# Kernel optimization log

Measured on AMD Instinct MI355X. Metric: run time of the kernel, lower is better.

The kernel has to match this reference:

```python
import jax, jax.numpy as jnp
import numpy as np

N_NODES = 64
KS = (52, 42, 34)  # ceil(0.8*64), ceil(0.8*52), ceil(0.8*42)


def _gcn(x, A, W, b):
    # GCNConv(improved=True): self-loop fill 2.0, symmetric normalization. A[tgt, src], weighted.
    n = A.shape[0]
    Ah = A + 2.0 * jnp.eye(n, dtype=A.dtype)
    d = Ah.sum(-1)
    dis = jnp.where(d > 0, jax.lax.rsqrt(d), 0.0)
    An = dis[:, None] * Ah * dis[None, :]
    return An @ (x @ W) + b


def _augment(A):
    # GraphUNet.augment_adj: add self loops (weight 1), A2 = A1 @ A1, remove self loops
    n = A.shape[0]
    eye = jnp.eye(n, dtype=A.dtype)
    A1 = A + eye
    return (A1 @ A1) * (1.0 - eye)


def _pool(x, A, w, k):
    # TopKPooling: score = tanh(x.w/||w||), keep top-k, scale kept features by score
    s = jnp.tanh((x @ w) / jnp.linalg.norm(w))
    sv, perm = jax.lax.top_k(s, k)
    return x[perm] * sv[:, None], A[perm][:, perm], perm


def _unet(x, A, dw0, db0, dws, dbs, pws, uws, ubs, uwl, ubl):
    # GraphUNet(depth=3, sum_res=True), single graph: x [n, F2], A [n, n]
    x = jax.nn.relu(_gcn(x, A, dw0, db0))
    xs, As, perms = [x], [A], []
    for i in range(3):
        A = _augment(A)
        x, A, perm = _pool(x, A, pws[i], KS[i])
        x = jax.nn.relu(_gcn(x, A, dws[i], dbs[i]))
        if i < 2:
            xs.append(x)
            As.append(A)
        perms.append(perm)
    for i in range(3):
        j = 2 - i
        res, Aj, perm = xs[j], As[j], perms[j]
        x = res + jnp.zeros_like(res).at[perm].set(x)
        if i < 2:
            x = jax.nn.relu(_gcn(x, Aj, uws[i], ubs[i]))
        else:
            x = _gcn(x, Aj, uwl, ubl)
    return x


def _nnconv(x, src, dst, ea, mw, mb, rw, bias):
    # NNConv(aggr='mean'): per-edge MLP weight, gather-matmul-scatter-mean + root + bias
    B, E = src.shape
    fin, fout = rw.shape
    We = jax.nn.relu(ea @ mw + mb).reshape(B, E, fin, fout)  # [B,E,fin,fout]
    xs = jnp.take_along_axis(x, src[..., None], axis=1)      # [B,E,fin]
    msg = jnp.einsum('bei,beio->beo', xs, We)                # [B,E,fout]
    seg = jax.vmap(lambda m, d: jax.ops.segment_sum(m, d, num_segments=N_NODES))
    sums = seg(msg, dst)
    cnt = seg(jnp.ones(msg.shape[:2] + (1,), msg.dtype), dst)
    agg = sums / jnp.maximum(cnt, 1.0)
    return agg + x @ rw + bias


def _adj(src, dst):
    A = jnp.zeros((N_NODES, N_NODES), jnp.float32).at[dst, src].set(1.0)
    return A * (1.0 - jnp.eye(N_NODES, dtype=jnp.float32))


def _branch(x, ei, ea, mlp1, mlp2, u1, u2):
    src, dst = ei[:, 0], ei[:, 1]
    A = jax.vmap(_adj)(src, dst)
    x = jax.nn.relu(_nnconv(x, src, dst, ea, *mlp1))
    x = jax.nn.relu(jax.vmap(lambda h, a: _unet(h, a, *u1))(x, A))
    x = jax.nn.relu(_nnconv(x, src, dst, ea, *mlp2))
    x = jax.nn.relu(jax.vmap(lambda h, a: _unet(h, a, *u2))(x, A))
    return x.mean(axis=1)  # global_mean_pool (equal-sized graphs)


def setup_inputs() -> dict:
    key = jax.random.key(0)
    keys = iter(jax.random.split(key, 64))
    def nrm(shape, s=1.0):
        return jax.random.normal(next(keys), shape, jnp.float32) * s
    B, n, E, F, F2, Q, H, C = 128, 64, 512, 64, 32, 16, 256, 50
    inp = {}
    inp['x1'] = nrm((B, n, F))
    inp['ei1'] = jax.random.randint(next(keys), (B, 2, E), 0, n, jnp.int32)
    inp['ea1'] = jax.random.uniform(next(keys), (B, E, 1), jnp.float32)
    inp['jw1'] = nrm((B, Q))
    inp['x2'] = nrm((B, n, F))
    inp['ei2'] = jax.random.randint(next(keys), (B, 2, E), 0, n, jnp.int32)
    inp['ea2'] = jax.random.uniform(next(keys), (B, E, 1), jnp.float32)
    inp['jw2'] = nrm((B, Q))
    inp['m1w'] = nrm((1, F * F2), 0.1)
    inp['m1b'] = nrm((F * F2,), 0.1)
    inp['r1w'] = nrm((F, F2), 0.1)
    inp['c1b'] = nrm((F2,), 0.1)
    inp['m2w'] = nrm((1, F2 * F2), 0.1)
    inp['m2b'] = nrm((F2 * F2,), 0.1)
    inp['r2w'] = nrm((F2, F2), 0.1)
    inp['c2b'] = nrm((F2,), 0.1)
    for p in ('u1', 'u2'):
        inp[p + '_dw0'] = nrm((F2, C), 0.1)
        inp[p + '_db0'] = nrm((C,), 0.1)
        inp[p + '_dws'] = nrm((3, C, C), 0.1)
        inp[p + '_dbs'] = nrm((3, C), 0.1)
        inp[p + '_pws'] = nrm((3, C), 0.1)
        inp[p + '_uws'] = nrm((2, C, C), 0.1)
        inp[p + '_ubs'] = nrm((2, C), 0.1)
        inp[p + '_uwl'] = nrm((C, F2), 0.1)
        inp[p + '_ubl'] = nrm((F2,), 0.1)
    inp['bb_w'] = nrm(((F2 + Q) * 2, H), 0.1)
    inp['bb_b'] = nrm((H,), 0.1)
    return inp


def reference(x1, ei1, ea1, jw1, x2, ei2, ea2, jw2,
              m1w, m1b, r1w, c1b, m2w, m2b, r2w, c2b,
              u1_dw0, u1_db0, u1_dws, u1_dbs, u1_pws, u1_uws, u1_ubs, u1_uwl, u1_ubl,
              u2_dw0, u2_db0, u2_dws, u2_dbs, u2_pws, u2_uws, u2_ubs, u2_uwl, u2_ubl,
              bb_w, bb_b):
    mlp1 = (m1w, m1b, r1w, c1b)
    mlp2 = (m2w, m2b, r2w, c2b)
    u1 = (u1_dw0, u1_db0, u1_dws, u1_dbs, u1_pws, u1_uws, u1_ubs, u1_uwl, u1_ubl)
    u2 = (u2_dw0, u2_db0, u2_dws, u2_dbs, u2_pws, u2_uws, u2_ubs, u2_uwl, u2_ubl)
    r1 = _branch(x1, ei1, ea1, mlp1, mlp2, u1, u2)
    r2 = _branch(x2, ei2, ea2, mlp1, mlp2, u1, u2)
    c = jnp.concatenate([r1, jw1, r2, jw2], axis=1)  # [(F2+Q)*2]
    return jax.nn.relu(c @ bb_w + bb_b)
```

## Files before the change

kernel.cpp:

```cpp
#include <hip/hip_runtime.h>
#include <math.h>

#define UT 1024
#define XS 52
#define ASTR 65

__device__ __forceinline__ float wred16(float v) {
    v += __shfl_xor(v, 8); v += __shfl_xor(v, 4);
    v += __shfl_xor(v, 2); v += __shfl_xor(v, 1);
    return v;
}

__global__ __launch_bounds__(256)
void adj_kernel(const int* __restrict__ eiA, const int* __restrict__ eiB,
                float* __restrict__ Aout)
{
    const int g = blockIdx.x, tid = threadIdx.x;
    const int* eig = (g < 128) ? (eiA + (size_t)g * 1024)
                               : (eiB + (size_t)(g - 128) * 1024);
    __shared__ float Al[4096];
    for (int i = tid; i < 4096; i += 256) Al[i] = 0.f;
    __syncthreads();
    for (int e = tid; e < 512; e += 256) {
        int s = eig[e], d = eig[512 + e];
        Al[d * 64 + s] = 1.f;
    }
    __syncthreads();
    if (tid < 64) Al[tid * 64 + tid] = 0.f;
    __syncthreads();
    for (int i = tid; i < 4096; i += 256) Aout[(size_t)g * 4096 + i] = Al[i];
}

template<int FIN>
__global__ __launch_bounds__(UT)
void nnconv_kernel(const float* __restrict__ xA, const float* __restrict__ xB,
                   const int* __restrict__ eiA, const int* __restrict__ eiB,
                   const float* __restrict__ eaA, const float* __restrict__ eaB,
                   const float* __restrict__ mw, const float* __restrict__ mb,
                   const float* __restrict__ rw, const float* __restrict__ bias,
                   float* __restrict__ out)
{
    constexpr int ICN = FIN / 16;
    constexpr int ERN = UT / (32 * ICN);
    constexpr int EPT = 512 / ERN;
    const int g = blockIdx.x, tid = threadIdx.x;
    const float* xg; const int* eig; const float* eag;
    if (g < 128) {
        xg = xA + (size_t)g * 64 * FIN; eig = eiA + (size_t)g * 1024; eag = eaA + (size_t)g * 512;
    } else {
        int h = g - 128;
        xg = xB + (size_t)h * 64 * FIN; eig = eiB + (size_t)h * 1024; eag = eaB + (size_t)h * 512;
    }

    __shared__ __align__(16) float xl[64 * FIN];
    __shared__ __align__(16) float mwl[FIN * 32];
    __shared__ __align__(16) float mbl[FIN * 32];
    __shared__ __align__(16) float rwl[FIN * 32];
    __shared__ __align__(16) float sums[64 * 32];
    __shared__ int   srcl[512];
    __shared__ int   dstl[512];
    __shared__ float eal[512];
    __shared__ float cntl[64];

    for (int i = tid; i < 64 * FIN; i += UT) xl[i] = xg[i];
    for (int i = tid; i < FIN * 32; i += UT) { mwl[i] = mw[i]; mbl[i] = mb[i]; rwl[i] = rw[i]; }
    for (int e = tid; e < 512; e += UT) {
        srcl[e] = eig[e]; dstl[e] = eig[512 + e]; eal[e] = eag[e];
    }
    for (int i = tid; i < 2048; i += UT) sums[i] = 0.f;
    if (tid < 64) cntl[tid] = 0.f;
    __syncthreads();

    const int o = tid & 31, ic = (tid >> 5) & (ICN - 1), er = tid / (32 * ICN);
    float mwr[16], mbr[16];
    #pragma unroll
    for (int z = 0; z < 16; z++) {
        mwr[z] = mwl[(ic * 16 + z) * 32 + o];
        mbr[z] = mbl[(ic * 16 + z) * 32 + o];
    }
    for (int e = tid; e < 512; e += UT) atomicAdd(&cntl[dstl[e]], 1.f);

    for (int e = er * EPT; e < er * EPT + EPT; e++) {
        int s = srcl[e]; int d = dstl[e]; float av = eal[e];
        float acc = 0.f;
        #pragma unroll
        for (int z = 0; z < 16; z += 4) {
            float4 xv = *(const float4*)&xl[s * FIN + ic * 16 + z];
            acc += xv.x * fmaxf(fmaf(av, mwr[z + 0], mbr[z + 0]), 0.f);
            acc += xv.y * fmaxf(fmaf(av, mwr[z + 1], mbr[z + 1]), 0.f);
            acc += xv.z * fmaxf(fmaf(av, mwr[z + 2], mbr[z + 2]), 0.f);
            acc += xv.w * fmaxf(fmaf(av, mwr[z + 3], mbr[z + 3]), 0.f);
        }
        acc += __shfl_down(acc, 32);
        if ((tid & 32) == 0) atomicAdd(&sums[d * 32 + o], acc);
    }
    __syncthreads();

    for (int it = tid; it < 512; it += UT) {
        int nn = it >> 3, o0 = (it & 7) * 4;
        float a0 = 0.f, a1 = 0.f, a2 = 0.f, a3 = 0.f;
        for (int i = 0; i < FIN; i++) {
            float xv = xl[nn * FIN + i];
            float4 w = *(const float4*)&rwl[i * 32 + o0];
            a0 = fmaf(xv, w.x, a0); a1 = fmaf(xv, w.y, a1);
            a2 = fmaf(xv, w.z, a2); a3 = fmaf(xv, w.w, a3);
        }
        float inv = 1.0f / fmaxf(cntl[nn], 1.f);
        float4 sv = *(const float4*)&sums[nn * 32 + o0];
        float4 bv = *(const float4*)&bias[o0];
        float4 r;
        r.x = fmaxf(sv.x * inv + a0 + bv.x, 0.f);
        r.y = fmaxf(sv.y * inv + a1 + bv.y, 0.f);
        r.z = fmaxf(sv.z * inv + a2 + bv.z, 0.f);
        r.w = fmaxf(sv.w * inv + a3 + bv.w, 0.f);
        *(float4*)&out[(size_t)g * 2048 + nn * 32 + o0] = r;
    }
}

__device__ __forceinline__ void gcn_u(int n, int cin, int cout,
    float* __restrict__ x, float* __restrict__ tmp,
    const float* __restrict__ A, float* __restrict__ Wl,
    float* __restrict__ dis,
    const float* __restrict__ Wg, const float* __restrict__ bg, bool relu)
{
    const int tid = threadIdx.x;
    const int nso = (cout + 3) >> 2;
    for (int idx = tid; idx < 51 * 52; idx += UT) {
        int r = idx / 52, c = idx - r * 52;
        float v = 0.f;
        if (r < cin && c < cout) v = Wg[r * cout + c];
        else if (r == 50 && c < cout) v = bg[c];
        Wl[idx] = v;
    }
    {
        int r = tid >> 4, l = tid & 15;
        float s = 0.f;
        if (r < n) for (int j = l; j < n; j += 16) s += A[r * ASTR + j];
        s = wred16(s);
        if (l == 0 && r < n) dis[r] = 1.0f / sqrtf(2.0f + s);
    }
    __syncthreads();
    int nr2 = n >> 1;
    for (int it = tid; it < nr2 * nso; it += UT) {
        int i0 = (it / nso) * 2, o0 = (it - (it / nso) * nso) * 4;
        float a0=0,a1=0,a2=0,a3=0, b0=0,b1=0,b2=0,b3=0;
        for (int k = 0; k < cin; k++) {
            float4 w = *(const float4*)&Wl[k * 52 + o0];
            float x0 = x[i0 * XS + k], x1 = x[(i0 + 1) * XS + k];
            a0 = fmaf(x0, w.x, a0); a1 = fmaf(x0, w.y, a1);
            a2 = fmaf(x0, w.z, a2); a3 = fmaf(x0, w.w, a3);
            b0 = fmaf(x1, w.x, b0); b1 = fmaf(x1, w.y, b1);
            b2 = fmaf(x1, w.z, b2); b3 = fmaf(x1, w.w, b3);
        }
        float d0 = dis[i0], d1 = dis[i0 + 1];
        float4 t0; t0.x = a0*d0; t0.y = a1*d0; t0.z = a2*d0; t0.w = a3*d0;
        float4 t1; t1.x = b0*d1; t1.y = b1*d1; t1.z = b2*d1; t1.w = b3*d1;
        *(float4*)&tmp[i0 * XS + o0] = t0;
        *(float4*)&tmp[(i0 + 1) * XS + o0] = t1;
    }
    __syncthreads();
    for (int it = tid; it < nr2 * nso; it += UT) {
        int i0 = (it / nso) * 2, o0 = (it - (it / nso) * nso) * 4;
        float a0=0,a1=0,a2=0,a3=0, b0=0,b1=0,b2=0,b3=0;
        for (int j = 0; j < n; j++) {
            float4 t = *(const float4*)&tmp[j * XS + o0];
            float av0 = A[i0 * ASTR + j], av1 = A[(i0 + 1) * ASTR + j];
            a0 = fmaf(av0, t.x, a0); a1 = fmaf(av0, t.y, a1);
            a2 = fmaf(av0, t.z, a2); a3 = fmaf(av0, t.w, a3);
            b0 = fmaf(av1, t.x, b0); b1 = fmaf(av1, t.y, b1);
            b2 = fmaf(av1, t.z, b2); b3 = fmaf(av1, t.w, b3);
        }
        float4 bias = *(const float4*)&Wl[50 * 52 + o0];
        float4 s0 = *(const float4*)&tmp[i0 * XS + o0];
        float4 s1 = *(const float4*)&tmp[(i0 + 1) * XS + o0];
        float d0 = dis[i0], d1 = dis[i0 + 1];
        float4 r0, r1;
        r0.x = fmaf(d0, a0 + 2.f*s0.x, bias.x); r0.y = fmaf(d0, a1 + 2.f*s0.y, bias.y);
        r0.z = fmaf(d0, a2 + 2.f*s0.z, bias.z); r0.w = fmaf(d0, a3 + 2.f*s0.w, bias.w);
        r1.x = fmaf(d1, b0 + 2.f*s1.x, bias.x); r1.y = fmaf(d1, b1 + 2.f*s1.y, bias.y);
        r1.z = fmaf(d1, b2 + 2.f*s1.z, bias.z); r1.w = fmaf(d1, b3 + 2.f*s1.w, bias.w);
        if (relu) {
            r0.x = fmaxf(r0.x, 0.f); r0.y = fmaxf(r0.y, 0.f);
            r0.z = fmaxf(r0.z, 0.f); r0.w = fmaxf(r0.w, 0.f);
            r1.x = fmaxf(r1.x, 0.f); r1.y = fmaxf(r1.y, 0.f);
            r1.z = fmaxf(r1.z, 0.f); r1.w = fmaxf(r1.w, 0.f);
        }
        *(float4*)&x[i0 * XS + o0] = r0;
        *(float4*)&x[(i0 + 1) * XS + o0] = r1;
    }
    __syncthreads();
}

__global__ __launch_bounds__(UT)
void unet_kernel(const float* __restrict__ xin, const float* __restrict__ Aglob,
                 const float* __restrict__ dw0, const float* __restrict__ db0,
                 const float* __restrict__ dws, const float* __restrict__ dbs,
                 const float* __restrict__ pws,
                 const float* __restrict__ uws, const float* __restrict__ ubs,
                 const float* __restrict__ uwl, const float* __restrict__ ubl,
                 float* __restrict__ ws_xs, float* __restrict__ ws_As,
                 float* __restrict__ outp, int mean_mode)
{
    const int g = blockIdx.x, tid = threadIdx.x;
    __shared__ __align__(16) float Aa[64 * ASTR];
    __shared__ __align__(16) float Ab[64 * ASTR];
    __shared__ __align__(16) float x0c[64 * XS];
    __shared__ __align__(16) float x1c[64 * XS];
    __shared__ float scr[64];
    __shared__ float dis[64];
    __shared__ float svals[64];
    __shared__ int   permL[192];

    float *pA = Aa, *pF = Ab, *px = x0c, *pt_ = x1c;
    float* xs_g = ws_xs + (size_t)g * 9984;
    float* as_g = ws_As + (size_t)g * 6144;
    const float* Ag_g = Aglob + (size_t)g * 4096;
    const int nsz[4] = {64, 52, 42, 34};

    {
        const float* xg = xin + (size_t)g * 2048;
        for (int idx = tid; idx < 512; idx += UT) {
            int i = idx >> 3, o0 = (idx & 7) * 4;
            *(float4*)&px[i * XS + o0] = *(const float4*)&xg[i * 32 + o0];
        }
        for (int idx = tid; idx < 4096; idx += UT)
            pA[(idx >> 6) * ASTR + (idx & 63)] = Ag_g[idx];
    }
    __syncthreads();

    gcn_u(64, 32, 50, px, pt_, pA, pF, dis, dw0, db0, true);

    for (int lvl = 0; lvl < 3; lvl++) {
        int n = nsz[lvl], kk = nsz[lvl + 1];
        const float* wg = pws + lvl * 50;
        int* perm = permL + lvl * 64;
        {
            int r = tid >> 4, l = tid & 15;
            float s = 0.f, wn = 0.f;
            for (int q = l; q < 50; q += 16) {
                float wv = wg[q];
                wn = fmaf(wv, wv, wn);
                s = fmaf(px[r * XS + q], wv, s);
            }
            s = wred16(s); wn = wred16(wn);
            if (l == 0 && r < n) scr[r] = tanhf(s / sqrtf(wn));
        }
        {
            float* xd = xs_g + lvl * 3328;
            for (int idx = tid; idx < 3328; idx += UT) xd[idx] = px[idx];
            if (lvl == 1) for (int idx = tid; idx < 52 * ASTR; idx += UT) as_g[idx] = pA[idx];
            if (lvl == 2) for (int idx = tid; idx < 42 * ASTR; idx += UT) as_g[3380 + idx] = pA[idx];
        }
        __syncthreads();
        if (tid < 64) {
            float v = (tid < n) ? scr[tid] : -2.0f;
            int id = tid;
            for (int sz = 2; sz <= 64; sz <<= 1)
                for (int st = sz >> 1; st > 0; st >>= 1) {
                    float ov = __shfl_xor(v, st);
                    int oi = __shfl_xor(id, st);
                    bool up = ((tid & sz) == 0);
                    bool lower = ((tid & st) == 0);
                    bool less = (v > ov) || (v == ov && id < oi);
                    bool keep = (up == lower) ? less : !less;
                    if (!keep) { v = ov; id = oi; }
                }
            if (tid < kk) { perm[tid] = id; svals[tid] = v; }
        }
        __syncthreads();
        for (int idx = tid; idx < n * 13; idx += UT) {
            int m = idx / 13, u0 = (idx - (idx / 13) * 13) * 4;
            float4 gv;
            gv.x = (u0 + 0 < kk) ? pA[m * ASTR + perm[u0 + 0]] : 0.f;
            gv.y = (u0 + 1 < kk) ? pA[m * ASTR + perm[u0 + 1]] : 0.f;
            gv.z = (u0 + 2 < kk) ? pA[m * ASTR + perm[u0 + 2]] : 0.f;
            gv.w = (u0 + 3 < kk) ? pA[m * ASTR + perm[u0 + 3]] : 0.f;
            *(float4*)&pt_[m * XS + u0] = gv;
        }
        float gx0=0, gx1=0, gx2=0, gx3=0; int gdst = -1;
        if (tid < kk * 13) {
            int t = tid / 13, q0 = (tid - t * 13) * 4;
            float sv = svals[t]; int p = perm[t];
            gx0 = px[p * XS + q0 + 0] * sv; gx1 = px[p * XS + q0 + 1] * sv;
            gx2 = px[p * XS + q0 + 2] * sv; gx3 = px[p * XS + q0 + 3] * sv;
            gdst = t * XS + q0;
        }
        __syncthreads();
        if (gdst >= 0) {
            px[gdst] = gx0; px[gdst + 1] = gx1; px[gdst + 2] = gx2; px[gdst + 3] = gx3;
        }
        int nt2 = kk >> 1, nst = (kk + 3) >> 2;
        for (int it = tid; it < nt2 * nst; it += UT) {
            int t0 = (it / nst) * 2, u0 = (it - (it / nst) * nst) * 4;
            int p0 = perm[t0], p1 = perm[t0 + 1];
            float a0=0,a1=0,a2=0,a3=0, b0=0,b1=0,b2=0,b3=0;
            for (int m = 0; m < n; m++) {
                float4 gv = *(const float4*)&pt_[m * XS + u0];
                float q0v = pA[p0 * ASTR + m], q1v = pA[p1 * ASTR + m];
                a0 = fmaf(q0v, gv.x, a0); a1 = fmaf(q0v, gv.y, a1);
                a2 = fmaf(q0v, gv.z, a2); a3 = fmaf(q0v, gv.w, a3);
                b0 = fmaf(q1v, gv.x, b0); b1 = fmaf(q1v, gv.y, b1);
                b2 = fmaf(q1v, gv.z, b2); b3 = fmaf(q1v, gv.w, b3);
            }
            float4 g0 = *(const float4*)&pt_[p0 * XS + u0];
            float4 g1 = *(const float4*)&pt_[p1 * XS + u0];
            float v;
            v = a0 + 2.f*g0.x; pF[t0*ASTR + u0+0] = (u0+0 == t0) ? 0.f : v;
            v = a1 + 2.f*g0.y; pF[t0*ASTR + u0+1] = (u0+1 == t0) ? 0.f : v;
            v = a2 + 2.f*g0.z; pF[t0*ASTR + u0+2] = (u0+2 == t0) ? 0.f : v;
            v = a3 + 2.f*g0.w; pF[t0*ASTR + u0+3] = (u0+3 == t0) ? 0.f : v;
            v = b0 + 2.f*g1.x; pF[(t0+1)*ASTR + u0+0] = (u0+0 == t0+1) ? 0.f : v;
            v = b1 + 2.f*g1.y; pF[(t0+1)*ASTR + u0+1] = (u0+1 == t0+1) ? 0.f : v;
            v = b2 + 2.f*g1.z; pF[(t0+1)*ASTR + u0+2] = (u0+2 == t0+1) ? 0.f : v;
            v = b3 + 2.f*g1.w; pF[(t0+1)*ASTR + u0+3] = (u0+3 == t0+1) ? 0.f : v;
        }
        __syncthreads();
        gcn_u(kk, 50, 50, px, pt_, pF, pA, dis, dws + lvl * 2500, dbs + lvl * 50, true);
        { float* t = pA; pA = pF; pF = t; }
    }

    for (int i2 = 0; i2 < 3; i2++) {
        int j = 2 - i2;
        int nj = nsz[j], kc = nsz[j + 1];
        {
            const float* resg = xs_g + j * 3328;
            for (int idx = tid; idx < 3328; idx += UT) pt_[idx] = resg[idx];
            if (j == 0) {
                for (int idx = tid; idx < 4096; idx += UT)
                    pF[(idx >> 6) * ASTR + (idx & 63)] = Ag_g[idx];
            } else if (j == 1) {
                for (int idx = tid; idx < 52 * ASTR; idx += UT) pF[idx] = as_g[idx];
            } else {
                for (int idx = tid; idx < 42 * ASTR; idx += UT) pF[idx] = as_g[3380 + idx];
            }
        }
        __syncthreads();
        const int* perm = permL + j * 64;
        for (int it = tid; it < kc * 13; it += UT) {
            int t = it / 13, q0 = (it - (it / 13) * 13) * 4;
            int p = perm[t];
            pt_[p * XS + q0 + 0] += px[t * XS + q0 + 0];
            pt_[p * XS + q0 + 1] += px[t * XS + q0 + 1];
            pt_[p * XS + q0 + 2] += px[t * XS + q0 + 2];
            pt_[p * XS + q0 + 3] += px[t * XS + q0 + 3];
        }
        __syncthreads();
        if (i2 < 2)
            gcn_u(nj, 50, 50, pt_, px, pF, pA, dis, uws + i2 * 2500, ubs + i2 * 50, true);
        else
            gcn_u(64, 50, 32, pt_, px, pF, pA, dis, uwl, ubl, false);
        { float* t2 = px; px = pt_; pt_ = t2; }
        { float* t2 = pA; pA = pF; pF = t2; }
    }

    if (mean_mode) {
        int r = tid >> 4, l = tid & 15;
        if (r < 32) {
            float s = 0.f;
            for (int i = l; i < 64; i += 16) s += fmaxf(px[i * XS + r], 0.f);
            s = wred16(s);
            if (l == 0) outp[(size_t)g * 32 + r] = s * (1.0f / 64.0f);
        }
    } else {
        float* og = outp + (size_t)g * 2048;
        for (int idx = tid; idx < 512; idx += UT) {
            int i = idx >> 3, o0 = (idx & 7) * 4;
            float4 vv = *(const float4*)&px[i * XS + o0];
            vv.x = fmaxf(vv.x, 0.f); vv.y = fmaxf(vv.y, 0.f);
            vv.z = fmaxf(vv.z, 0.f); vv.w = fmaxf(vv.w, 0.f);
            *(float4*)&og[i * 32 + o0] = vv;
        }
    }
}

__global__ __launch_bounds__(256)
void head_kernel(const float* __restrict__ r,
                 const float* __restrict__ jw1, const float* __restrict__ jw2,
                 const float* __restrict__ bw, const float* __restrict__ bb,
                 float* __restrict__ out)
{
    const int b = blockIdx.x, h = threadIdx.x;
    float acc = bb[h];
    const float* r1 = r + (size_t)b * 32;
    const float* r2 = r + (size_t)(128 + b) * 32;
    #pragma unroll
    for (int q = 0; q < 32; q++) acc += r1[q] * bw[q * 256 + h];
    #pragma unroll
    for (int q = 0; q < 16; q++) acc += jw1[b * 16 + q] * bw[(32 + q) * 256 + h];
    #pragma unroll
    for (int q = 0; q < 32; q++) acc += r2[q] * bw[(48 + q) * 256 + h];
    #pragma unroll
    for (int q = 0; q < 16; q++) acc += jw2[b * 16 + q] * bw[(80 + q) * 256 + h];
    out[(size_t)b * 256 + h] = fmaxf(acc, 0.f);
}

extern "C" void kernel_launch(void* const* d_in, const int* in_sizes, int n_in,
                              void* d_out, int out_size, void* d_ws, size_t ws_size,
                              hipStream_t stream)
{
    const float* x1  = (const float*)d_in[0];
    const int*   ei1 = (const int*)  d_in[1];
    const float* ea1 = (const float*)d_in[2];
    const float* jw1 = (const float*)d_in[3];
    const float* x2  = (const float*)d_in[4];
    const int*   ei2 = (const int*)  d_in[5];
    const float* ea2 = (const float*)d_in[6];
    const float* jw2 = (const float*)d_in[7];
    const float* m1w = (const float*)d_in[8];
    const float* m1b = (const float*)d_in[9];
    const float* r1w = (const float*)d_in[10];
    const float* c1b = (const float*)d_in[11];
    const float* m2w = (const float*)d_in[12];
    const float* m2b = (const float*)d_in[13];
    const float* r2w = (const float*)d_in[14];
    const float* c2b = (const float*)d_in[15];
    const float* u1p[9]; for (int i = 0; i < 9; i++) u1p[i] = (const float*)d_in[16 + i];
    const float* u2p[9]; for (int i = 0; i < 9; i++) u2p[i] = (const float*)d_in[25 + i];
    const float* bbw = (const float*)d_in[34];
    const float* bbb = (const float*)d_in[35];

    char* ws = (char*)d_ws;
    size_t off = 0;
    float* A    = (float*)(ws + off); off += 256ull * 4096 * 4;
    float* xc1  = (float*)(ws + off); off += 256ull * 2048 * 4;
    float* xu1  = (float*)(ws + off); off += 256ull * 2048 * 4;
    float* xc2  = (float*)(ws + off); off += 256ull * 2048 * 4;
    float* rr   = (float*)(ws + off); off += 256ull * 32 * 4;
    float* wxs  = (float*)(ws + off); off += 256ull * 9984 * 4;
    float* wAs  = (float*)(ws + off); off += 256ull * 6144 * 4;
    (void)ws_size; (void)in_sizes; (void)n_in; (void)out_size;

    adj_kernel<<<256, 256, 0, stream>>>(ei1, ei2, A);
    nnconv_kernel<64><<<256, UT, 0, stream>>>(x1, x2, ei1, ei2, ea1, ea2,
                                              m1w, m1b, r1w, c1b, xc1);
    unet_kernel<<<256, UT, 0, stream>>>(xc1, A,
        u1p[0], u1p[1], u1p[2], u1p[3], u1p[4], u1p[5], u1p[6], u1p[7], u1p[8],
        wxs, wAs, xu1, 0);
    nnconv_kernel<32><<<256, UT, 0, stream>>>(xu1, xu1 + 128ull * 2048,
                                              ei1, ei2, ea1, ea2,
                                              m2w, m2b, r2w, c2b, xc2);
    unet_kernel<<<256, UT, 0, stream>>>(xc2, A,
        u2p[0], u2p[1], u2p[2], u2p[3], u2p[4], u2p[5], u2p[6], u2p[7], u2p[8],
        wxs, wAs, rr, 1);
    head_kernel<<<128, 256, 0, stream>>>(rr, jw1, jw2, bbw, bbb, (float*)d_out);
}
```

Before: 358.4 us.

## Fuse adjacency, NNConv and both UNets into one persistent per-graph kernel

Replaces the five kernels (adjacency build, two NNConvs, two UNets) with a single kernel per graph that keeps features and adjacency in shared memory across phases. Skip-connection features and pooled adjacencies are held in registers instead of being spilled to global workspace, and the padded adjacency is written once to global memory for reload. This is meant to remove launch gaps and the global round-trips between stages. In exchange it raises register pressure, which may spill, and puts a long serial chain in each block with one block per graph.

```diff
diff --git a/kernel.cpp b/kernel.cpp
--- a/kernel.cpp
+++ b/kernel.cpp
@@ -9,112 +9,6 @@
     v += __shfl_xor(v, 8); v += __shfl_xor(v, 4);
     v += __shfl_xor(v, 2); v += __shfl_xor(v, 1);
     return v;
-}
-
-__global__ __launch_bounds__(256)
-void adj_kernel(const int* __restrict__ eiA, const int* __restrict__ eiB,
-                float* __restrict__ Aout)
-{
-    const int g = blockIdx.x, tid = threadIdx.x;
-    const int* eig = (g < 128) ? (eiA + (size_t)g * 1024)
-                               : (eiB + (size_t)(g - 128) * 1024);
-    __shared__ float Al[4096];
-    for (int i = tid; i < 4096; i += 256) Al[i] = 0.f;
-    __syncthreads();
-    for (int e = tid; e < 512; e += 256) {
-        int s = eig[e], d = eig[512 + e];
-        Al[d * 64 + s] = 1.f;
-    }
-    __syncthreads();
-    if (tid < 64) Al[tid * 64 + tid] = 0.f;
-    __syncthreads();
-    for (int i = tid; i < 4096; i += 256) Aout[(size_t)g * 4096 + i] = Al[i];
-}
-
-template<int FIN>
-__global__ __launch_bounds__(UT)
-void nnconv_kernel(const float* __restrict__ xA, const float* __restrict__ xB,
-                   const int* __restrict__ eiA, const int* __restrict__ eiB,
-                   const float* __restrict__ eaA, const float* __restrict__ eaB,
-                   const float* __restrict__ mw, const float* __restrict__ mb,
-                   const float* __restrict__ rw, const float* __restrict__ bias,
-                   float* __restrict__ out)
-{
-    constexpr int ICN = FIN / 16;
-    constexpr int ERN = UT / (32 * ICN);
-    constexpr int EPT = 512 / ERN;
-    const int g = blockIdx.x, tid = threadIdx.x;
-    const float* xg; const int* eig; const float* eag;
-    if (g < 128) {
-        xg = xA + (size_t)g * 64 * FIN; eig = eiA + (size_t)g * 1024; eag = eaA + (size_t)g * 512;
-    } else {
-        int h = g - 128;
-        xg = xB + (size_t)h * 64 * FIN; eig = eiB + (size_t)h * 1024; eag = eaB + (size_t)h * 512;
-    }
-
-    __shared__ __align__(16) float xl[64 * FIN];
-    __shared__ __align__(16) float mwl[FIN * 32];
-    __shared__ __align__(16) float mbl[FIN * 32];
-    __shared__ __align__(16) float rwl[FIN * 32];
-    __shared__ __align__(16) float sums[64 * 32];
-    __shared__ int   srcl[512];
-    __shared__ int   dstl[512];
-    __shared__ float eal[512];
-    __shared__ float cntl[64];
-
-    for (int i = tid; i < 64 * FIN; i += UT) xl[i] = xg[i];
-    for (int i = tid; i < FIN * 32; i += UT) { mwl[i] = mw[i]; mbl[i] = mb[i]; rwl[i] = rw[i]; }
-    for (int e = tid; e < 512; e += UT) {
-        srcl[e] = eig[e]; dstl[e] = eig[512 + e]; eal[e] = eag[e];
-    }
-    for (int i = tid; i < 2048; i += UT) sums[i] = 0.f;
-    if (tid < 64) cntl[tid] = 0.f;
-    __syncthreads();
-
-    const int o = tid & 31, ic = (tid >> 5) & (ICN - 1), er = tid / (32 * ICN);
-    float mwr[16], mbr[16];
-    #pragma unroll
-    for (int z = 0; z < 16; z++) {
-        mwr[z] = mwl[(ic * 16 + z) * 32 + o];
-        mbr[z] = mbl[(ic * 16 + z) * 32 + o];
-    }
-    for (int e = tid; e < 512; e += UT) atomicAdd(&cntl[dstl[e]], 1.f);
-
-    for (int e = er * EPT; e < er * EPT + EPT; e++) {
-        int s = srcl[e]; int d = dstl[e]; float av = eal[e];
-        float acc = 0.f;
-        #pragma unroll
-        for (int z = 0; z < 16; z += 4) {
-            float4 xv = *(const float4*)&xl[s * FIN + ic * 16 + z];
-            acc += xv.x * fmaxf(fmaf(av, mwr[z + 0], mbr[z + 0]), 0.f);
-            acc += xv.y * fmaxf(fmaf(av, mwr[z + 1], mbr[z + 1]), 0.f);
-            acc += xv.z * fmaxf(fmaf(av, mwr[z + 2], mbr[z + 2]), 0.f);
-            acc += xv.w * fmaxf(fmaf(av, mwr[z + 3], mbr[z + 3]), 0.f);
-        }
-        acc += __shfl_down(acc, 32);
-        if ((tid & 32) == 0) atomicAdd(&sums[d * 32 + o], acc);
-    }
-    __syncthreads();
-
-    for (int it = tid; it < 512; it += UT) {
-        int nn = it >> 3, o0 = (it & 7) * 4;
-        float a0 = 0.f, a1 = 0.f, a2 = 0.f, a3 = 0.f;
-        for (int i = 0; i < FIN; i++) {
-            float xv = xl[nn * FIN + i];
-            float4 w = *(const float4*)&rwl[i * 32 + o0];
-            a0 = fmaf(xv, w.x, a0); a1 = fmaf(xv, w.y, a1);
-            a2 = fmaf(xv, w.z, a2); a3 = fmaf(xv, w.w, a3);
-        }
-        float inv = 1.0f / fmaxf(cntl[nn], 1.f);
-        float4 sv = *(const float4*)&sums[nn * 32 + o0];
-        float4 bv = *(const float4*)&bias[o0];
-        float4 r;
-        r.x = fmaxf(sv.x * inv + a0 + bv.x, 0.f);
-        r.y = fmaxf(sv.y * inv + a1 + bv.y, 0.f);
-        r.z = fmaxf(sv.z * inv + a2 + bv.z, 0.f);
-        r.w = fmaxf(sv.w * inv + a3 + bv.w, 0.f);
-        *(float4*)&out[(size_t)g * 2048 + nn * 32 + o0] = r;
-    }
 }
 
 __device__ __forceinline__ void gcn_u(int n, int cin, int cout,
@@ -191,186 +85,335 @@
     __syncthreads();
 }
 
-__global__ __launch_bounds__(UT)
-void unet_kernel(const float* __restrict__ xin, const float* __restrict__ Aglob,
-                 const float* __restrict__ dw0, const float* __restrict__ db0,
-                 const float* __restrict__ dws, const float* __restrict__ dbs,
-                 const float* __restrict__ pws,
-                 const float* __restrict__ uws, const float* __restrict__ ubs,
-                 const float* __restrict__ uwl, const float* __restrict__ ubl,
-                 float* __restrict__ ws_xs, float* __restrict__ ws_As,
-                 float* __restrict__ outp, int mean_mode)
-{
-    const int g = blockIdx.x, tid = threadIdx.x;
-    __shared__ __align__(16) float Aa[64 * ASTR];
-    __shared__ __align__(16) float Ab[64 * ASTR];
-    __shared__ __align__(16) float x0c[64 * XS];
-    __shared__ __align__(16) float x1c[64 * XS];
-    __shared__ float scr[64];
-    __shared__ float dis[64];
-    __shared__ float svals[64];
-    __shared__ int   permL[192];
-
-    float *pA = Aa, *pF = Ab, *px = x0c, *pt_ = x1c;
-    float* xs_g = ws_xs + (size_t)g * 9984;
-    float* as_g = ws_As + (size_t)g * 6144;
-    const float* Ag_g = Aglob + (size_t)g * 4096;
-    const int nsz[4] = {64, 52, 42, 34};
-
+template<int FIN>
+__device__ __forceinline__ void nnconv_phase(
+    const float* __restrict__ xl, float* __restrict__ sums,
+    const int* __restrict__ srcl, const int* __restrict__ dstl,
+    const float* __restrict__ eal, float* __restrict__ cnt,
+    float* __restrict__ rwl,
+    const float* __restrict__ mw, const float* __restrict__ mb,
+    const float* __restrict__ rw, const float* __restrict__ bias,
+    float* __restrict__ xout)
+{
+    const int tid = threadIdx.x;
+    constexpr int ICN = FIN / 16;
+    constexpr int ERN = UT / (32 * ICN);
+    constexpr int EPT = 512 / ERN;
+    for (int i = tid; i < 2048; i += UT) sums[i] = 0.f;
+    for (int i = tid; i < FIN * 32; i += UT) rwl[i] = rw[i];
+    if (tid < 64) cnt[tid] = 0.f;
+    const int o = tid & 31, ic = (tid >> 5) & (ICN - 1), er = tid / (32 * ICN);
+    float mwr[16], mbr[16];
+    #pragma unroll
+    for (int z = 0; z < 16; z++) {
+        mwr[z] = mw[(ic * 16 + z) * 32 + o];
+        mbr[z] = mb[(ic * 16 + z) * 32 + o];
+    }
+    __syncthreads();
+    for (int e = tid; e < 512; e += UT) atomicAdd(&cnt[dstl[e]], 1.f);
+    for (int e = er * EPT; e < er * EPT + EPT; e++) {
+        int s = srcl[e]; int d = dstl[e]; float av = eal[e];
+        float acc = 0.f;
+        #pragma unroll
+        for (int z = 0; z < 16; z += 4) {
+            float4 xv = *(const float4*)&xl[s * FIN + ic * 16 + z];
+            acc += xv.x * fmaxf(fmaf(av, mwr[z + 0], mbr[z + 0]), 0.f);
+            acc += xv.y * fmaxf(fmaf(av, mwr[z + 1], mbr[z + 1]), 0.f);
+            acc += xv.z * fmaxf(fmaf(av, mwr[z + 2], mbr[z + 2]), 0.f);
+            acc += xv.w * fmaxf(fmaf(av, mwr[z + 3], mbr[z + 3]), 0.f);
+        }
+        acc += __shfl_down(acc, 32);
+        if ((tid & 32) == 0) atomicAdd(&sums[d * 32 + o], acc);
+    }
+    __syncthreads();
     {
-        const float* xg = xin + (size_t)g * 2048;
-        for (int idx = tid; idx < 512; idx += UT) {
-            int i = idx >> 3, o0 = (idx & 7) * 4;
-            *(float4*)&px[i * XS + o0] = *(const float4*)&xg[i * 32 + o0];
-        }
-        for (int idx = tid; idx < 4096; idx += UT)
-            pA[(idx >> 6) * ASTR + (idx & 63)] = Ag_g[idx];
-    }
-    __syncthreads();
+        int nn = tid >> 4, o0 = (tid & 15) * 2;
+        float a0 = 0.f, a1 = 0.f;
+        for (int i = 0; i < FIN; i++) {
+            float xv = xl[nn * FIN + i];
+            float2 w = *(const float2*)&rwl[i * 32 + o0];
+            a0 = fmaf(xv, w.x, a0); a1 = fmaf(xv, w.y, a1);
+        }
+        float inv = 1.0f / fmaxf(cnt[nn], 1.f);
+        float2 sv = *(const float2*)&sums[nn * 32 + o0];
+        xout[nn * XS + o0]     = fmaxf(fmaf(sv.x, inv, a0 + bias[o0]),     0.f);
+        xout[nn * XS + o0 + 1] = fmaxf(fmaf(sv.y, inv, a1 + bias[o0 + 1]), 0.f);
+    }
+    __syncthreads();
+}
+
+__device__ __forceinline__ void down_scores(int n, const float* __restrict__ wg,
+                                            const float* __restrict__ px,
+                                            float* __restrict__ scr)
+{
+    const int tid = threadIdx.x;
+    int r = tid >> 4, l = tid & 15;
+    float s = 0.f, wn = 0.f;
+    for (int q = l; q < 50; q += 16) {
+        float wv = wg[q];
+        wn = fmaf(wv, wv, wn);
+        s  = fmaf(px[r * XS + q], wv, s);
+    }
+    s = wred16(s); wn = wred16(wn);
+    if (l == 0 && r < n) scr[r] = tanhf(s / sqrtf(wn));
+}
+
+__device__ __forceinline__ void down_rest(int n, int kk,
+    float* __restrict__ px, float* __restrict__ pt_,
+    float* __restrict__ pA, float* __restrict__ pF,
+    float* __restrict__ scr, float* __restrict__ dis, float* __restrict__ svals,
+    int* __restrict__ perm, const float* __restrict__ dw,
+    const float* __restrict__ db)
+{
+    const int tid = threadIdx.x;
+    __syncthreads();
+    if (tid < 64) {
+        float v = (tid < n) ? scr[tid] : -2.0f;
+        int id = tid;
+        for (int sz = 2; sz <= 64; sz <<= 1)
+            for (int st = sz >> 1; st > 0; st >>= 1) {
+                float ov = __shfl_xor(v, st);
+                int oi = __shfl_xor(id, st);
+                bool up = ((tid & sz) == 0);
+                bool lower = ((tid & st) == 0);
+                bool less = (v > ov) || (v == ov && id < oi);
+                bool keep = (up == lower) ? less : !less;
+                if (!keep) { v = ov; id = oi; }
+            }
+        if (tid < kk) { perm[tid] = id; svals[tid] = v; }
+    }
+    __syncthreads();
+    for (int idx = tid; idx < n * 13; idx += UT) {
+        int m = idx / 13, u0 = (idx - (idx / 13) * 13) * 4;
+        float4 gv;
+        gv.x = (u0 + 0 < kk) ? pA[m * ASTR + perm[u0 + 0]] : 0.f;
+        gv.y = (u0 + 1 < kk) ? pA[m * ASTR + perm[u0 + 1]] : 0.f;
+        gv.z = (u0 + 2 < kk) ? pA[m * ASTR + perm[u0 + 2]] : 0.f;
+        gv.w = (u0 + 3 < kk) ? pA[m * ASTR + perm[u0 + 3]] : 0.f;
+        *(float4*)&pt_[m * XS + u0] = gv;
+    }
+    float gx0=0, gx1=0, gx2=0, gx3=0; int gdst = -1;
+    if (tid < kk * 13) {
+        int t = tid / 13, q0 = (tid - t * 13) * 4;
+        float sv = svals[t]; int p = perm[t];
+        gx0 = px[p * XS + q0 + 0] * sv; gx1 = px[p * XS + q0 + 1] * sv;
+        gx2 = px[p * XS + q0 + 2] * sv; gx3 = px[p * XS + q0 + 3] * sv;
+        gdst = t * XS + q0;
+    }
+    __syncthreads();
+    if (gdst >= 0) {
+        px[gdst] = gx0; px[gdst + 1] = gx1; px[gdst + 2] = gx2; px[gdst + 3] = gx3;
+    }
+    int nt2 = kk >> 1, nst = (kk + 3) >> 2;
+    for (int it = tid; it < nt2 * nst; it += UT) {
+        int t0 = (it / nst) * 2, u0 = (it - (it / nst) * nst) * 4;
+        int p0 = perm[t0], p1 = perm[t0 + 1];
+        float a0=0,a1=0,a2=0,a3=0, b0=0,b1=0,b2=0,b3=0;
+        for (int m = 0; m < n; m++) {
+            float4 gv = *(const float4*)&pt_[m * XS + u0];
+            float q0v = pA[p0 * ASTR + m], q1v = pA[p1 * ASTR + m];
+            a0 = fmaf(q0v, gv.x, a0); a1 = fmaf(q0v, gv.y, a1);
+            a2 = fmaf(q0v, gv.z, a2); a3 = fmaf(q0v, gv.w, a3);
+            b0 = fmaf(q1v, gv.x, b0); b1 = fmaf(q1v, gv.y, b1);
+            b2 = fmaf(q1v, gv.z, b2); b3 = fmaf(q1v, gv.w, b3);
+        }
+        float4 g0 = *(const float4*)&pt_[p0 * XS + u0];
+        float4 g1 = *(const float4*)&pt_[p1 * XS + u0];
+        float v;
+        v = a0 + 2.f*g0.x; pF[t0*ASTR + u0+0] = (u0+0 == t0) ? 0.f : v;
+        v = a1 + 2.f*g0.y; pF[t0*ASTR + u0+1] = (u0+1 == t0) ? 0.f : v;
+        v = a2 + 2.f*g0.z; pF[t0*ASTR + u0+2] = (u0+2 == t0) ? 0.f : v;
+        v = a3 + 2.f*g0.w; pF[t0*ASTR + u0+3] = (u0+3 == t0) ? 0.f : v;
+        v = b0 + 2.f*g1.x; pF[(t0+1)*ASTR + u0+0] = (u0+0 == t0+1) ? 0.f : v;
+        v = b1 + 2.f*g1.y; pF[(t0+1)*ASTR + u0+1] = (u0+1 == t0+1) ? 0.f : v;
+        v = b2 + 2.f*g1.z; pF[(t0+1)*ASTR + u0+2] = (u0+2 == t0+1) ? 0.f : v;
+        v = b3 + 2.f*g1.w; pF[(t0+1)*ASTR + u0+3] = (u0+3 == t0+1) ? 0.f : v;
+    }
+    __syncthreads();
+    gcn_u(kk, 50, 50, px, pt_, pF, pA, dis, dw, db, true);
+}
+
+__device__ __forceinline__ void unet_run(
+    float* __restrict__ Aa, float* __restrict__ Ab,
+    float* __restrict__ xa, float* __restrict__ xb,
+    float* __restrict__ scr, float* __restrict__ dis, float* __restrict__ svals,
+    int* __restrict__ permL, const float* __restrict__ wsAg,
+    const float* __restrict__ dw0, const float* __restrict__ db0,
+    const float* __restrict__ dws, const float* __restrict__ dbs,
+    const float* __restrict__ pws, const float* __restrict__ uws,
+    const float* __restrict__ ubs, const float* __restrict__ uwl,
+    const float* __restrict__ ubl,
+    float* __restrict__ outp, int g, int mean_mode)
+{
+    const int tid = threadIdx.x;
+    for (int i = tid; i < 4160; i += UT) Aa[i] = wsAg[i];
+    __syncthreads();
+    float *pA = Aa, *pF = Ab, *px = xa, *pt_ = xb;
 
     gcn_u(64, 32, 50, px, pt_, pA, pF, dis, dw0, db0, true);
 
-    for (int lvl = 0; lvl < 3; lvl++) {
-        int n = nsz[lvl], kk = nsz[lvl + 1];
-        const float* wg = pws + lvl * 50;
-        int* perm = permL + lvl * 64;
-        {
-            int r = tid >> 4, l = tid & 15;
-            float s = 0.f, wn = 0.f;
-            for (int q = l; q < 50; q += 16) {
-                float wv = wg[q];
-                wn = fmaf(wv, wv, wn);
-                s = fmaf(px[r * XS + q], wv, s);
-            }
-            s = wred16(s); wn = wred16(wn);
-            if (l == 0 && r < n) scr[r] = tanhf(s / sqrtf(wn));
-        }
-        {
-            float* xd = xs_g + lvl * 3328;
-            for (int idx = tid; idx < 3328; idx += UT) xd[idx] = px[idx];
-            if (lvl == 1) for (int idx = tid; idx < 52 * ASTR; idx += UT) as_g[idx] = pA[idx];
-            if (lvl == 2) for (int idx = tid; idx < 42 * ASTR; idx += UT) as_g[3380 + idx] = pA[idx];
-        }
-        __syncthreads();
-        if (tid < 64) {
-            float v = (tid < n) ? scr[tid] : -2.0f;
-            int id = tid;
-            for (int sz = 2; sz <= 64; sz <<= 1)
-                for (int st = sz >> 1; st > 0; st >>= 1) {
-                    float ov = __shfl_xor(v, st);
-                    int oi = __shfl_xor(id, st);
-                    bool up = ((tid & sz) == 0);
-                    bool lower = ((tid & st) == 0);
-                    bool less = (v > ov) || (v == ov && id < oi);
-                    bool keep = (up == lower) ? less : !less;
-                    if (!keep) { v = ov; id = oi; }
-                }
-            if (tid < kk) { perm[tid] = id; svals[tid] = v; }
-        }
-        __syncthreads();
-        for (int idx = tid; idx < n * 13; idx += UT) {
-            int m = idx / 13, u0 = (idx - (idx / 13) * 13) * 4;
-            float4 gv;
-            gv.x = (u0 + 0 < kk) ? pA[m * ASTR + perm[u0 + 0]] : 0.f;
-            gv.y = (u0 + 1 < kk) ? pA[m * ASTR + perm[u0 + 1]] : 0.f;
-            gv.z = (u0 + 2 < kk) ? pA[m * ASTR + perm[u0 + 2]] : 0.f;
-            gv.w = (u0 + 3 < kk) ? pA[m * ASTR + perm[u0 + 3]] : 0.f;
-            *(float4*)&pt_[m * XS + u0] = gv;
-        }
-        float gx0=0, gx1=0, gx2=0, gx3=0; int gdst = -1;
-        if (tid < kk * 13) {
-            int t = tid / 13, q0 = (tid - t * 13) * 4;
-            float sv = svals[t]; int p = perm[t];
-            gx0 = px[p * XS + q0 + 0] * sv; gx1 = px[p * XS + q0 + 1] * sv;
-            gx2 = px[p * XS + q0 + 2] * sv; gx3 = px[p * XS + q0 + 3] * sv;
-            gdst = t * XS + q0;
-        }
-        __syncthreads();
-        if (gdst >= 0) {
-            px[gdst] = gx0; px[gdst + 1] = gx1; px[gdst + 2] = gx2; px[gdst + 3] = gx3;
-        }
-        int nt2 = kk >> 1, nst = (kk + 3) >> 2;
-        for (int it = tid; it < nt2 * nst; it += UT) {
-            int t0 = (it / nst) * 2, u0 = (it - (it / nst) * nst) * 4;
-            int p0 = perm[t0], p1 = perm[t0 + 1];
-            float a0=0,a1=0,a2=0,a3=0, b0=0,b1=0,b2=0,b3=0;
-            for (int m = 0; m < n; m++) {
-                float4 gv = *(const float4*)&pt_[m * XS + u0];
-                float q0v = pA[p0 * ASTR + m], q1v = pA[p1 * ASTR + m];
-                a0 = fmaf(q0v, gv.x, a0); a1 = fmaf(q0v, gv.y, a1);
-                a2 = fmaf(q0v, gv.z, a2); a3 = fmaf(q0v, gv.w, a3);
-                b0 = fmaf(q1v, gv.x, b0); b1 = fmaf(q1v, gv.y, b1);
-                b2 = fmaf(q1v, gv.z, b2); b3 = fmaf(q1v, gv.w, b3);
-            }
-            float4 g0 = *(const float4*)&pt_[p0 * XS + u0];
-            float4 g1 = *(const float4*)&pt_[p1 * XS + u0];
-            float v;
-            v = a0 + 2.f*g0.x; pF[t0*ASTR + u0+0] = (u0+0 == t0) ? 0.f : v;
-            v = a1 + 2.f*g0.y; pF[t0*ASTR + u0+1] = (u0+1 == t0) ? 0.f : v;
-            v = a2 + 2.f*g0.z; pF[t0*ASTR + u0+2] = (u0+2 == t0) ? 0.f : v;
-            v = a3 + 2.f*g0.w; pF[t0*ASTR + u0+3] = (u0+3 == t0) ? 0.f : v;
-            v = b0 + 2.f*g1.x; pF[(t0+1)*ASTR + u0+0] = (u0+0 == t0+1) ? 0.f : v;
-            v = b1 + 2.f*g1.y; pF[(t0+1)*ASTR + u0+1] = (u0+1 == t0+1) ? 0.f : v;
-            v = b2 + 2.f*g1.z; pF[(t0+1)*ASTR + u0+2] = (u0+2 == t0+1) ? 0.f : v;
-            v = b3 + 2.f*g1.w; pF[(t0+1)*ASTR + u0+3] = (u0+3 == t0+1) ? 0.f : v;
-        }
-        __syncthreads();
-        gcn_u(kk, 50, 50, px, pt_, pF, pA, dis, dws + lvl * 2500, dbs + lvl * 50, true);
-        { float* t = pA; pA = pF; pF = t; }
-    }
-
-    for (int i2 = 0; i2 < 3; i2++) {
-        int j = 2 - i2;
-        int nj = nsz[j], kc = nsz[j + 1];
-        {
-            const float* resg = xs_g + j * 3328;
-            for (int idx = tid; idx < 3328; idx += UT) pt_[idx] = resg[idx];
-            if (j == 0) {
-                for (int idx = tid; idx < 4096; idx += UT)
-                    pF[(idx >> 6) * ASTR + (idx & 63)] = Ag_g[idx];
-            } else if (j == 1) {
-                for (int idx = tid; idx < 52 * ASTR; idx += UT) pF[idx] = as_g[idx];
-            } else {
-                for (int idx = tid; idx < 42 * ASTR; idx += UT) pF[idx] = as_g[3380 + idx];
-            }
-        }
-        __syncthreads();
-        const int* perm = permL + j * 64;
-        for (int it = tid; it < kc * 13; it += UT) {
-            int t = it / 13, q0 = (it - (it / 13) * 13) * 4;
-            int p = perm[t];
-            pt_[p * XS + q0 + 0] += px[t * XS + q0 + 0];
-            pt_[p * XS + q0 + 1] += px[t * XS + q0 + 1];
-            pt_[p * XS + q0 + 2] += px[t * XS + q0 + 2];
-            pt_[p * XS + q0 + 3] += px[t * XS + q0 + 3];
-        }
-        __syncthreads();
-        if (i2 < 2)
-            gcn_u(nj, 50, 50, pt_, px, pF, pA, dis, uws + i2 * 2500, ubs + i2 * 50, true);
-        else
-            gcn_u(64, 50, 32, pt_, px, pF, pA, dis, uwl, ubl, false);
-        { float* t2 = px; px = pt_; pt_ = t2; }
-        { float* t2 = pA; pA = pF; pF = t2; }
-    }
+    down_scores(64, pws, px, scr);
+    float xs0_0 = px[tid], xs0_1 = px[tid+1024], xs0_2 = px[tid+2048];
+    float xs0_3 = (tid < 256) ? px[tid+3072] : 0.f;
+    down_rest(64, 52, px, pt_, pA, pF, scr, dis, svals, permL, dws, dbs);
+    { float* t = pA; pA = pF; pF = t; }
+
+    down_scores(52, pws + 50, px, scr);
+    float xs1_0 = px[tid], xs1_1 = px[tid+1024], xs1_2 = px[tid+2048];
+    float xs1_3 = (tid < 256) ? px[tid+3072] : 0.f;
+    float A1_0 = pA[tid], A1_1 = pA[tid+1024], A1_2 = pA[tid+2048];
+    float A1_3 = (tid < 308) ? pA[tid+3072] : 0.f;
+    down_rest(52, 42, px, pt_, pA, pF, scr, dis, svals, permL + 64,
+              dws + 2500, dbs + 50);
+    { float* t = pA; pA = pF; pF = t; }
+
+    down_scores(42, pws + 100, px, scr);
+    float xs2_0 = px[tid], xs2_1 = px[tid+1024], xs2_2 = px[tid+2048];
+    float xs2_3 = (tid < 256) ? px[tid+3072] : 0.f;
+    float A2_0 = pA[tid], A2_1 = pA[tid+1024];
+    float A2_2 = (tid < 682) ? pA[tid+2048] : 0.f;
+    down_rest(42, 34, px, pt_, pA, pF, scr, dis, svals, permL + 128,
+              dws + 5000, dbs + 100);
+    { float* t = pA; pA = pF; pF = t; }
+
+    pt_[tid] = xs2_0; pt_[tid+1024] = xs2_1; pt_[tid+2048] = xs2_2;
+    if (tid < 256) pt_[tid+3072] = xs2_3;
+    pF[tid] = A2_0; pF[tid+1024] = A2_1;
+    if (tid < 682) pF[tid+2048] = A2_2;
+    __syncthreads();
+    for (int it = tid; it < 34 * 13; it += UT) {
+        int t = it / 13, q0 = (it - t * 13) * 4;
+        int p = permL[128 + t];
+        pt_[p*XS+q0+0] += px[t*XS+q0+0]; pt_[p*XS+q0+1] += px[t*XS+q0+1];
+        pt_[p*XS+q0+2] += px[t*XS+q0+2]; pt_[p*XS+q0+3] += px[t*XS+q0+3];
+    }
+    __syncthreads();
+    gcn_u(42, 50, 50, pt_, px, pF, pA, dis, uws, ubs, true);
+    { float* t = px; px = pt_; pt_ = t; t = pA; pA = pF; pF = t; }
+
+    pt_[tid] = xs1_0; pt_[tid+1024] = xs1_1; pt_[tid+2048] = xs1_2;
+    if (tid < 256) pt_[tid+3072] = xs1_3;
+    pF[tid] = A1_0; pF[tid+1024] = A1_1; pF[tid+2048] = A1_2;
+    if (tid < 308) pF[tid+3072] = A1_3;
+    __syncthreads();
+    for (int it = tid; it < 42 * 13; it += UT) {
+        int t = it / 13, q0 = (it - t * 13) * 4;
+        int p = permL[64 + t];
+        pt_[p*XS+q0+0] += px[t*XS+q0+0]; pt_[p*XS+q0+1] += px[t*XS+q0+1];
+        pt_[p*XS+q0+2] += px[t*XS+q0+2]; pt_[p*XS+q0+3] += px[t*XS+q0+3];
+    }
+    __syncthreads();
+    gcn_u(52, 50, 50, pt_, px, pF, pA, dis, uws + 2500, ubs + 50, true);
+    { float* t = px; px = pt_; pt_ = t; t = pA; pA = pF; pF = t; }
+
+    pt_[tid] = xs0_0; pt_[tid+1024] = xs0_1; pt_[tid+2048] = xs0_2;
+    if (tid < 256) pt_[tid+3072] = xs0_3;
+    for (int i = tid; i < 4160; i += UT) pF[i] = wsAg[i];
+    __syncthreads();
+    for (int it = tid; it < 52 * 13; it += UT) {
+        int t = it / 13, q0 = (it - t * 13) * 4;
+        int p = permL[t];
+        pt_[p*XS+q0+0] += px[t*XS+q0+0]; pt_[p*XS+q0+1] += px[t*XS+q0+1];
+        pt_[p*XS+q0+2] += px[t*XS+q0+2]; pt_[p*XS+q0+3] += px[t*XS+q0+3];
+    }
+    __syncthreads();
+    gcn_u(64, 50, 32, pt_, px, pF, pA, dis, uwl, ubl, false);
 
     if (mean_mode) {
         int r = tid >> 4, l = tid & 15;
         if (r < 32) {
             float s = 0.f;
-            for (int i = l; i < 64; i += 16) s += fmaxf(px[i * XS + r], 0.f);
+            for (int i = l; i < 64; i += 16) s += fmaxf(xb[i * XS + r], 0.f);
             s = wred16(s);
             if (l == 0) outp[(size_t)g * 32 + r] = s * (1.0f / 64.0f);
         }
+        __syncthreads();
+    }
+}
+
+__global__ __launch_bounds__(UT)
+void fused_kernel(
+    const float* __restrict__ x1, const float* __restrict__ x2,
+    const int* __restrict__ ei1, const int* __restrict__ ei2,
+    const float* __restrict__ ea1, const float* __restrict__ ea2,
+    const float* __restrict__ m1w, const float* __restrict__ m1b,
+    const float* __restrict__ r1w, const float* __restrict__ c1b,
+    const float* __restrict__ m2w, const float* __restrict__ m2b,
+    const float* __restrict__ r2w, const float* __restrict__ c2b,
+    const float* __restrict__ u1_0, const float* __restrict__ u1_1,
+    const float* __restrict__ u1_2, const float* __restrict__ u1_3,
+    const float* __restrict__ u1_4, const float* __restrict__ u1_5,
+    const float* __restrict__ u1_6, const float* __restrict__ u1_7,
+    const float* __restrict__ u1_8,
+    const float* __restrict__ u2_0, const float* __restrict__ u2_1,
+    const float* __restrict__ u2_2, const float* __restrict__ u2_3,
+    const float* __restrict__ u2_4, const float* __restrict__ u2_5,
+    const float* __restrict__ u2_6, const float* __restrict__ u2_7,
+    const float* __restrict__ u2_8,
+    float* __restrict__ wsA, float* __restrict__ rr)
+{
+    const int g = blockIdx.x, tid = threadIdx.x;
+    __shared__ __align__(16) float smem[15424];
+    float* Aa    = smem;
+    float* Ab    = smem + 4160;
+    float* xa    = smem + 8320;
+    float* xb    = smem + 11648;
+    float* scr   = smem + 14976;
+    float* dis   = smem + 15040;
+    float* svals = smem + 15104;
+    int*   permL = (int*)(smem + 15168);
+    float* cnt   = smem + 15360;
+    float* xl   = Aa;
+    float* sums = Ab;
+    int*   srcl = (int*)(Ab + 2048);
+    int*   dstl = (int*)(Ab + 2560);
+    float* eal  = Ab + 3072;
+
+    float* wsAg = wsA + (size_t)g * 4160;
+    const int* eig; const float* eag; const float* xg;
+    if (g < 128) {
+        eig = ei1 + (size_t)g * 1024; eag = ea1 + (size_t)g * 512;
+        xg = x1 + (size_t)g * 4096;
     } else {
-        float* og = outp + (size_t)g * 2048;
-        for (int idx = tid; idx < 512; idx += UT) {
-            int i = idx >> 3, o0 = (idx & 7) * 4;
-            float4 vv = *(const float4*)&px[i * XS + o0];
-            vv.x = fmaxf(vv.x, 0.f); vv.y = fmaxf(vv.y, 0.f);
-            vv.z = fmaxf(vv.z, 0.f); vv.w = fmaxf(vv.w, 0.f);
-            *(float4*)&og[i * 32 + o0] = vv;
-        }
-    }
+        int h = g - 128;
+        eig = ei2 + (size_t)h * 1024; eag = ea2 + (size_t)h * 512;
+        xg = x2 + (size_t)h * 4096;
+    }
+
+    for (int e = tid; e < 512; e += UT) {
+        srcl[e] = eig[e]; dstl[e] = eig[512 + e]; eal[e] = eag[e];
+    }
+    for (int i = tid; i < 4160; i += UT) Aa[i] = 0.f;
+    __syncthreads();
+    for (int e = tid; e < 512; e += UT) Aa[dstl[e] * ASTR + srcl[e]] = 1.f;
+    __syncthreads();
+    if (tid < 64) Aa[tid * ASTR + tid] = 0.f;
+    __syncthreads();
+    for (int i = tid; i < 4160; i += UT) wsAg[i] = Aa[i];
+    __threadfence_block();
+    __syncthreads();
+
+    for (int i = tid; i < 4096; i += UT) xl[i] = xg[i];
+    __syncthreads();
+    nnconv_phase<64>(xl, sums, srcl, dstl, eal, cnt, xb, m1w, m1b, r1w, c1b, xa);
+
+    unet_run(Aa, Ab, xa, xb, scr, dis, svals, permL, wsAg,
+             u1_0, u1_1, u1_2, u1_3, u1_4, u1_5, u1_6, u1_7, u1_8,
+             nullptr, g, 0);
+
+    for (int idx = tid; idx < 2048; idx += UT) {
+        int i = idx >> 5, o = idx & 31;
+        xl[idx] = fmaxf(xb[i * XS + o], 0.f);
+    }
+    for (int e = tid; e < 512; e += UT) {
+        srcl[e] = eig[e]; dstl[e] = eig[512 + e]; eal[e] = eag[e];
+    }
+    __syncthreads();
+    nnconv_phase<32>(xl, sums, srcl, dstl, eal, cnt, xb, m2w, m2b, r2w, c2b, xa);
+
+    unet_run(Aa, Ab, xa, xb, scr, dis, svals, permL, wsAg,
+             u2_0, u2_1, u2_2, u2_3, u2_4, u2_5, u2_6, u2_7, u2_8,
+             rr, g, 1);
 }
 
 __global__ __launch_bounds__(256)
@@ -420,27 +463,15 @@
     const float* bbb = (const float*)d_in[35];
 
     char* ws = (char*)d_ws;
-    size_t off = 0;
-    float* A    = (float*)(ws + off); off += 256ull * 4096 * 4;
-    float* xc1  = (float*)(ws + off); off += 256ull * 2048 * 4;
-    float* xu1  = (float*)(ws + off); off += 256ull * 2048 * 4;
-    float* xc2  = (float*)(ws + off); off += 256ull * 2048 * 4;
-    float* rr   = (float*)(ws + off); off += 256ull * 32 * 4;
-    float* wxs  = (float*)(ws + off); off += 256ull * 9984 * 4;
-    float* wAs  = (float*)(ws + off); off += 256ull * 6144 * 4;
+    float* wsA = (float*)ws;
+    float* rr  = (float*)(ws + 256ull * 4160 * 4);
     (void)ws_size; (void)in_sizes; (void)n_in; (void)out_size;
 
-    adj_kernel<<<256, 256, 0, stream>>>(ei1, ei2, A);
-    nnconv_kernel<64><<<256, UT, 0, stream>>>(x1, x2, ei1, ei2, ea1, ea2,
-                                              m1w, m1b, r1w, c1b, xc1);
-    unet_kernel<<<256, UT, 0, stream>>>(xc1, A,
+    fused_kernel<<<256, UT, 0, stream>>>(
+        x1, x2, ei1, ei2, ea1, ea2,
+        m1w, m1b, r1w, c1b, m2w, m2b, r2w, c2b,
         u1p[0], u1p[1], u1p[2], u1p[3], u1p[4], u1p[5], u1p[6], u1p[7], u1p[8],
-        wxs, wAs, xu1, 0);
-    nnconv_kernel<32><<<256, UT, 0, stream>>>(xu1, xu1 + 128ull * 2048,
-                                              ei1, ei2, ea1, ea2,
-                                              m2w, m2b, r2w, c2b, xc2);
-    unet_kernel<<<256, UT, 0, stream>>>(xc2, A,
         u2p[0], u2p[1], u2p[2], u2p[3], u2p[4], u2p[5], u2p[6], u2p[7], u2p[8],
-        wxs, wAs, rr, 1);
+        wsA, rr);
     head_kernel<<<128, 256, 0, stream>>>(rr, jw1, jw2, bbw, bbb, (float*)d_out);
 }
```

Result: slower. 461.3 us (+28.7%).
